# Kernel optimization log

Measured on AMD Instinct MI355X. Metric: run time of the kernel, lower is better.

Reference implementation:

```python
import jax, jax.numpy as jnp
import numpy as np

S, L, T, E, H = 512, 5, 20, 768, 64


def setup_inputs() -> dict:
    key = jax.random.key(0)
    ks = jax.random.split(key, 32)

    def p(k, shape, scale=0.05):
        return jax.random.normal(k, shape, dtype=jnp.float32) * scale

    return {
        "text_input": jax.random.normal(ks[0], (S, L, T, E), dtype=jnp.float32),
        "time_inputs": jax.random.uniform(ks[1], (S, L, T), dtype=jnp.float32),
        # TimeLSTM per-stock params (gate order f, i, o, c_tmp)
        "Wall": p(ks[2], (S, H, 4 * H)), "bWall": p(ks[3], (S, 4 * H)),
        "Uall": p(ks[4], (S, E, 4 * H)), "bUall": p(ks[5], (S, 4 * H)),
        "Wd": p(ks[6], (S, H, H)), "bWd": p(ks[7], (S, H)),
        # shared text/day Attention per stock
        "W1": p(ks[8], (S, H, H)), "b1": p(ks[9], (S, H)),
        "W2": p(ks[10], (S, H, H)), "b2": p(ks[11], (S, H)),
        "V": p(ks[12], (S, H, 1)), "bV": p(ks[13], (S, 1)),
        # day nn.LSTM per stock (gate order i, f, g, o)
        "Wih": p(ks[14], (S, H, 4 * H)), "Whh": p(ks[15], (S, H, 4 * H)),
        "bih": p(ks[16], (S, 4 * H)), "bhh": p(ks[17], (S, 4 * H)),
        # shared output head
        "lin_w": p(ks[18], (H, 1)), "lin_b": p(ks[19], (1,)),
        "no_stocks": S,
    }


def _forward(text_input, time_inputs, Wall, bWall, Uall, bUall, Wd, bWd,
             W1, b1, W2, b2, V, bV, Wih, Whh, bih, bhh, lin_w, lin_b, no_stocks):
    def per_stock(x, ts, Wall, bWall, Uall, bUall, Wd, bWd,
                  W1, b1, W2, b2, V, bV, Wih, Whh, bih, bhh):
        # x: [L, T, E], ts: [L, T] -- lookback days are an inner batch for the TimeLSTM
        u = jnp.einsum('lte,eg->ltg', x, Uall) + bUall  # [L, T, 4H]

        def step(carry, inp):
            h, c = carry                 # [L, H]
            u_t, ts_t = inp              # [L, 4H], [L]
            c_s1 = jnp.tanh(c @ Wd + bWd)
            c_adj = (c - c_s1) + c_s1 * ts_t[:, None]
            gates = h @ Wall + bWall + u_t
            f, i, o, c_tmp = jnp.split(gates, 4, axis=1)
            f = jax.nn.sigmoid(f)
            i = jax.nn.sigmoid(i)
            o = jax.nn.sigmoid(o)
            c_tmp = jax.nn.sigmoid(c_tmp)  # sigmoid (not tanh), faithful to source
            c_new = f * c_adj + i * c_tmp
            h_new = o * jnp.tanh(c_new)
            return (h_new, c_new), o     # module collects the o gate as 'outputs'

        init = (jnp.zeros((L, H), x.dtype), jnp.zeros((L, H), x.dtype))
        (h_fin, _), o_seq = jax.lax.scan(step, init, (u.transpose(1, 0, 2), ts.T))
        full = o_seq.transpose(1, 0, 2)  # [L, T, H]

        # text attention: score = V(tanh(W1(last) + W2(full))), softmax over T
        score = jnp.tanh((h_fin @ W1 + b1)[:, None, :] + full @ W2 + b2) @ V + bV  # [L, T, 1]
        aw = jax.nn.softmax(score, axis=1)
        text_vec = jnp.sum(aw * full, axis=1)  # [L, H]

        # day nn.LSTM: input (1, L, H) seq-first => one cell step with batch=L, zero state
        h0 = jnp.zeros((L, H), x.dtype)
        g = text_vec @ Wih + bih + h0 @ Whh + bhh
        gi, gf, gg, go = jnp.split(g, 4, axis=1)
        c_d = jax.nn.sigmoid(gi) * jnp.tanh(gg)  # f * c0 = 0
        h_d = jax.nn.sigmoid(go) * jnp.tanh(c_d)  # [L, H]; output == h_n here

        # day attention reuses the SAME text_attention weights; full == last == h_d
        s2 = jnp.tanh(h_d @ W1 + b1 + h_d @ W2 + b2) @ V + bV  # [L, 1]
        aw2 = jax.nn.softmax(s2, axis=0)
        return jnp.sum(aw2 * h_d, axis=0)  # [H]

    ft_vec = jax.vmap(per_stock)(text_input, time_inputs, Wall, bWall, Uall, bUall,
                                 Wd, bWd, W1, b1, W2, b2, V, bV,
                                 Wih, Whh, bih, bhh)  # [S, H]
    return jax.nn.leaky_relu(ft_vec @ lin_w + lin_b, negative_slope=0.01)  # [S, 1]


def reference(text_input, time_inputs, Wall, bWall, Uall, bUall, Wd, bWd,
              W1, b1, W2, b2, V, bV, Wih, Whh, bih, bhh, lin_w, lin_b, no_stocks):
    return _forward(text_input, time_inputs, Wall, bWall, Uall, bUall, Wd, bWd,
                    W1, b1, W2, b2, V, bV, Wih, Whh, bih, bhh, lin_w, lin_b, no_stocks)
```

## Files before the change

### kernel.cpp

```cpp
#include <hip/hip_runtime.h>
#include <cstddef>

#define NS 512
#define NL 5
#define NT 20
#define NE 768
#define NH 64
#define NG 256

__device__ __forceinline__ float sigf(float x) { return 1.0f / (1.0f + expf(-x)); }

typedef __fp16 h16x2 __attribute__((ext_vector_type(2)));
typedef _Float16 f16x8 __attribute__((ext_vector_type(8)));
typedef __attribute__((ext_vector_type(4))) float f32x4;

union PkU { h16x2 h; unsigned u; };
union U16 { __fp16 f; unsigned short s; };

__device__ __forceinline__ void split_pk(float a, float b, unsigned& hi, unsigned& lo) {
    PkU H, L;
    H.h = __builtin_amdgcn_cvt_pkrtz(a, b);
    float ra = a - (float)H.h[0];
    float rb = b - (float)H.h[1];
    L.h = __builtin_amdgcn_cvt_pkrtz(ra, rb);
    hi = H.u; lo = L.u;
}

__device__ __forceinline__ void pack8(const float v[8], uint4& ph, uint4& pl) {
    split_pk(v[0], v[1], ph.x, pl.x);
    split_pk(v[2], v[3], ph.y, pl.y);
    split_pk(v[4], v[5], ph.z, pl.z);
    split_pk(v[6], v[7], ph.w, pl.w);
}

__device__ __forceinline__ void stage8(const float v[8], unsigned short* base, unsigned off) {
    uint4 ph, pl;
    pack8(v, ph, pl);
    *(uint4*)&base[off]       = ph;
    *(uint4*)&base[off + 512] = pl;
}

__global__ __launch_bounds__(512, 4) void k_gemm_u(
    const float* __restrict__ x, const float* __restrict__ U,
    const float* __restrict__ bU, float* __restrict__ u)
{
    __shared__ unsigned short Af[8 * 2 * 512];
    __shared__ unsigned short Bf[8 * 2 * 512];
    const int bid = blockIdx.x;
    const int s = bid >> 1, half = bid & 1;
    const int tid = threadIdx.x;
    const int wave = tid >> 6, lane = tid & 63;
    const int wm = wave & 1, wn = wave >> 1;
    const float* xg = x + (size_t)s * (NL * NT * NE);
    const float* Ug = U + (size_t)s * (NE * NG) + half * 128;

    f32x4 acc[4][2] = {};

    const int arow = tid >> 2, ab = tid & 3;
    const unsigned a_off = ((unsigned)(arow >> 4) * 2) * 512 + ((arow & 15) + 16 * ab) * 8;
    const int bcol = tid & 127, bkq = tid >> 7;
    const unsigned b_off = ((unsigned)(bcol >> 4) * 2) * 512 + ((bcol & 15) + 16 * bkq) * 8;

    float av[8], bv[8];
    {
        const float* pa = xg + (size_t)arow * NE + ab * 8;
        if (arow < 100) {
            float4 q0 = *(const float4*)pa, q1 = *(const float4*)(pa + 4);
            av[0]=q0.x; av[1]=q0.y; av[2]=q0.z; av[3]=q0.w;
            av[4]=q1.x; av[5]=q1.y; av[6]=q1.z; av[7]=q1.w;
        } else {
            #pragma unroll
            for (int j = 0; j < 8; ++j) av[j] = 0.0f;
        }
        #pragma unroll
        for (int j = 0; j < 8; ++j)
            bv[j] = Ug[(size_t)(8 * bkq + j) * NG + bcol];
    }

    for (int st = 0; st < 24; ++st) {
        stage8(av, Af, a_off);
        stage8(bv, Bf, b_off);
        __syncthreads();

        if (st + 1 < 24) {
            const int k0 = (st + 1) * 32;
            const float* pa = xg + (size_t)arow * NE + k0 + ab * 8;
            if (arow < 100) {
                float4 q0 = *(const float4*)pa, q1 = *(const float4*)(pa + 4);
                av[0]=q0.x; av[1]=q0.y; av[2]=q0.z; av[3]=q0.w;
                av[4]=q1.x; av[5]=q1.y; av[6]=q1.z; av[7]=q1.w;
            } else {
                #pragma unroll
                for (int j = 0; j < 8; ++j) av[j] = 0.0f;
            }
            #pragma unroll
            for (int j = 0; j < 8; ++j)
                bv[j] = Ug[(size_t)(k0 + 8 * bkq + j) * NG + bcol];
        }

        f16x8 bh[2], bl[2];
        #pragma unroll
        for (int ni = 0; ni < 2; ++ni) {
            const unsigned nt = wn * 2 + ni;
            bh[ni] = *(const f16x8*)&Bf[(nt * 2 + 0) * 512 + lane * 8];
            bl[ni] = *(const f16x8*)&Bf[(nt * 2 + 1) * 512 + lane * 8];
        }
        #pragma unroll
        for (int mi = 0; mi < 4; ++mi) {
            const unsigned mt = wm * 4 + mi;
            f16x8 ah = *(const f16x8*)&Af[(mt * 2 + 0) * 512 + lane * 8];
            f16x8 al = *(const f16x8*)&Af[(mt * 2 + 1) * 512 + lane * 8];
            #pragma unroll
            for (int ni = 0; ni < 2; ++ni) {
                acc[mi][ni] = __builtin_amdgcn_mfma_f32_16x16x32_f16(ah, bh[ni], acc[mi][ni], 0, 0, 0);
                acc[mi][ni] = __builtin_amdgcn_mfma_f32_16x16x32_f16(ah, bl[ni], acc[mi][ni], 0, 0, 0);
                acc[mi][ni] = __builtin_amdgcn_mfma_f32_16x16x32_f16(al, bh[ni], acc[mi][ni], 0, 0, 0);
            }
        }
        __syncthreads();
    }

    const int c_sub = 4 * (lane >> 4);
    #pragma unroll
    for (int ni = 0; ni < 2; ++ni) {
        const int gcol = half * 128 + (wn * 2 + ni) * 16 + (lane & 15);
        const float bb = bU[(size_t)s * NG + gcol];
        #pragma unroll
        for (int mi = 0; mi < 4; ++mi) {
            const int grow0 = wm * 64 + mi * 16 + c_sub;
            #pragma unroll
            for (int r = 0; r < 4; ++r) {
                const int grow = grow0 + r;
                if (grow < 100) {
                    const int ld = grow / 20, td = grow % 20;
                    u[(((size_t)s * NT + td) * NL + ld) * NG + gcol] = acc[mi][ni][r] + bb;
                }
            }
        }
    }
}

#define RSTRIDE 72

__global__ __launch_bounds__(512, 4) void k_recur(
    float* __restrict__ u, const float* __restrict__ ti,
    const float* __restrict__ Wall, const float* __restrict__ bWall,
    const float* __restrict__ Wd, const float* __restrict__ bWd)
{
    __shared__ float GATES[NL * NG];
    __shared__ float WDC[NL * NH];
    __shared__ unsigned short HSH[16 * RSTRIDE];
    __shared__ unsigned short HSL[16 * RSTRIDE];
    __shared__ unsigned short CSH[16 * RSTRIDE];
    __shared__ unsigned short CSL[16 * RSTRIDE];
    __shared__ float TSH[NL * NT];

    const int s = blockIdx.x;
    const int tid = threadIdx.x;
    const int wave = tid >> 6, lane = tid & 63;
    float* ug = u + (size_t)s * NT * NL * NG;

    for (int i = tid; i < 16 * RSTRIDE; i += 512) {
        HSH[i] = 0; HSL[i] = 0; CSH[i] = 0; CSL[i] = 0;
    }
    if (tid < NL * NT) TSH[tid] = ti[(size_t)s * NL * NT + tid];

    const int nT = (wave < 4) ? 3 : 2;
    f16x8 Bh[3][2], Bl[3][2];
    {
        const float* Wg = Wall + (size_t)s * (NH * NG);
        const float* Dg = Wd + (size_t)s * (NH * NH);
        const int fcol = lane & 15, foct = lane >> 4;
        #pragma unroll
        for (int t2 = 0; t2 < 3; ++t2) {
            if (t2 < nT) {
                const int tc = wave + t2 * 8;
                #pragma unroll
                for (int ks = 0; ks < 2; ++ks) {
                    float v[8];
                    if (tc < 16) {
                        #pragma unroll
                        for (int j = 0; j < 8; ++j)
                            v[j] = Wg[(size_t)(ks * 32 + foct * 8 + j) * NG + tc * 16 + fcol];
                    } else {
                        #pragma unroll
                        for (int j = 0; j < 8; ++j)
                            v[j] = Dg[(size_t)(ks * 32 + foct * 8 + j) * NH + (tc - 16) * 16 + fcol];
                    }
                    union { uint4 u4; f16x8 h8; } H, L;
                    pack8(v, H.u4, L.u4);
                    Bh[t2][ks] = H.h8;
                    Bl[t2][ks] = L.h8;
                }
            }
        }
    }

    const int lq = tid >> 6, hh = tid & 63;
    float bw[4], bwd_r = 0.0f, un[4], c_reg = 0.0f, h_reg = 0.0f;
    if (tid < 320) {
        #pragma unroll
        for (int j = 0; j < 4; ++j) {
            bw[j] = bWall[(size_t)s * NG + j * 64 + hh];
            un[j] = ug[(size_t)(0 * NL + lq) * NG + j * 64 + hh];
        }
        bwd_r = bWd[(size_t)s * NH + hh];
    }
    __syncthreads();

    const int arow = lane & 15, akq = lane >> 4;
    const unsigned afrag0 = (unsigned)arow * RSTRIDE + akq * 8;
    const unsigned afrag1 = afrag0 + 32;
    for (int t = 0; t < NT; ++t) {
        f16x8 ah[2], al[2];
        ah[0] = *(const f16x8*)&HSH[afrag0];
        ah[1] = *(const f16x8*)&HSH[afrag1];
        al[0] = *(const f16x8*)&HSL[afrag0];
        al[1] = *(const f16x8*)&HSL[afrag1];
        f16x8 cah[2], cal[2];
        if (wave < 4) {
            cah[0] = *(const f16x8*)&CSH[afrag0];
            cah[1] = *(const f16x8*)&CSH[afrag1];
            cal[0] = *(const f16x8*)&CSL[afrag0];
            cal[1] = *(const f16x8*)&CSL[afrag1];
        }
        #pragma unroll
        for (int t2 = 0; t2 < 3; ++t2) {
            if (t2 < nT) {
                const int tc = wave + t2 * 8;
                const bool isWd = (tc >= 16);
                f32x4 acc = {};
                #pragma unroll
                for (int ks = 0; ks < 2; ++ks) {
                    f16x8 A_h = isWd ? cah[ks] : ah[ks];
                    f16x8 A_l = isWd ? cal[ks] : al[ks];
                    acc = __builtin_amdgcn_mfma_f32_16x16x32_f16(A_h, Bh[t2][ks], acc, 0, 0, 0);
                    acc = __builtin_amdgcn_mfma_f32_16x16x32_f16(A_h, Bl[t2][ks], acc, 0, 0, 0);
                    acc = __builtin_amdgcn_mfma_f32_16x16x32_f16(A_l, Bh[t2][ks], acc, 0, 0, 0);
                }
                #pragma unroll
                for (int r = 0; r < 4; ++r) {
                    const int row = 4 * akq + r;
                    if (row < NL) {
                        if (!isWd) GATES[row * NG + tc * 16 + arow] = acc[r];
                        else       WDC[row * NH + (tc - 16) * 16 + arow] = acc[r];
                    }
                }
            }
        }
        float unx[4];
        if (tid < 320 && t + 1 < NT) {
            #pragma unroll
            for (int j = 0; j < 4; ++j)
                unx[j] = ug[(size_t)((t + 1) * NL + lq) * NG + j * 64 + hh];
        }
        __syncthreads();

        if (tid < 320) {
            float g0 = GATES[lq * NG + hh]        + bw[0] + un[0];
            float g1 = GATES[lq * NG + 64 + hh]   + bw[1] + un[1];
            float g2 = GATES[lq * NG + 128 + hh]  + bw[2] + un[2];
            float g3 = GATES[lq * NG + 192 + hh]  + bw[3] + un[3];
            float f  = sigf(g0), ii = sigf(g1), oo = sigf(g2), ct = sigf(g3);
            float cs1 = tanhf(WDC[lq * NH + hh] + bwd_r);
            float ca  = c_reg - cs1 + cs1 * TSH[lq * NT + t];
            float cn  = f * ca + ii * ct;
            c_reg = cn;
            h_reg = oo * tanhf(cn);
            const unsigned sidx = (unsigned)lq * RSTRIDE + hh;
            U16 a, b;
            a.f = (__fp16)h_reg;            HSH[sidx] = a.s;
            b.f = (__fp16)(h_reg - (float)a.f); HSL[sidx] = b.s;
            a.f = (__fp16)cn;               CSH[sidx] = a.s;
            b.f = (__fp16)(cn - (float)a.f);   CSL[sidx] = b.s;
            ug[(size_t)(t * NL + lq) * NG + hh] = oo;
            #pragma unroll
            for (int j = 0; j < 4; ++j) un[j] = unx[j];
        }
        __syncthreads();
    }
    if (tid < 320)
        ug[(size_t)(0 * NL + lq) * NG + 64 + hh] = h_reg;
}

#define P_W1    0
#define P_W2    4096
#define P_FULLO 8192
#define P_HS    14592
#define P_TQ    14912
#define P_CA    15232
#define P_SC    15552
#define P_B0    15652
#define P_B1    15716
#define P_BVV   15780
#define P_BV1   15844
#define P_TOT   15848

__global__ __launch_bounds__(320, 2) void k_post(
    const float* __restrict__ u,
    const float* __restrict__ W1, const float* __restrict__ b1,
    const float* __restrict__ W2, const float* __restrict__ b2,
    const float* __restrict__ V, const float* __restrict__ bV,
    const float* __restrict__ Wih, const float* __restrict__ bih,
    const float* __restrict__ bhh, const float* __restrict__ lin_w,
    const float* __restrict__ lin_b, float* __restrict__ out)
{
    __shared__ float sm[P_TOT];
    const int s = blockIdx.x;
    const int tid = threadIdx.x;
    const int lq = tid >> 6, hh = tid & 63;
    const int lane = hh;
    const float* ug = u + (size_t)s * NT * NL * NG;

    for (int i = tid; i < 1024; i += 320)
        *(float4*)&sm[P_W1 + i * 4] = *(const float4*)(W1 + (size_t)s * 4096 + i * 4);
    for (int i = tid; i < 1024; i += 320)
        *(float4*)&sm[P_W2 + i * 4] = *(const float4*)(W2 + (size_t)s * 4096 + i * 4);
    for (int i = tid; i < 1600; i += 320) {
        const int idx = i >> 4;
        const int l = idx / NT, t = idx % NT;
        const int k4 = (i & 15) * 4;
        *(float4*)&sm[P_FULLO + idx * NH + k4] =
            *(const float4*)(ug + (size_t)(t * NL + l) * NG + k4);
    }
    sm[P_HS + tid] = ug[(size_t)(0 * NL + lq) * NG + 64 + hh];
    if (tid < NH) {
        sm[P_B0 + tid]  = b1[(size_t)s * NH + tid];
        sm[P_B1 + tid]  = b2[(size_t)s * NH + tid];
        sm[P_BVV + tid] = V[(size_t)s * NH + tid];
    }
    if (tid == 0) sm[P_BV1] = bV[s];
    __syncthreads();

    {
        float qv = sm[P_B0 + hh];
        for (int k4 = 0; k4 < NH; k4 += 4) {
            float4 hv = *(const float4*)&sm[P_HS + lq * NH + k4];
            qv += hv.x * sm[P_W1 + (k4 + 0) * NH + hh]
                + hv.y * sm[P_W1 + (k4 + 1) * NH + hh]
                + hv.z * sm[P_W1 + (k4 + 2) * NH + hh]
                + hv.w * sm[P_W1 + (k4 + 3) * NH + hh];
        }
        sm[P_TQ + tid] = qv;
    }
    __syncthreads();

    for (int lt = lq; lt < NL * NT; lt += 5) {
        int l = lt / NT;
        float v = sm[P_TQ + l * NH + lane] + sm[P_B1 + lane];
        for (int k4 = 0; k4 < NH; k4 += 4) {
            float4 fv = *(const float4*)&sm[P_FULLO + lt * NH + k4];
            v += fv.x * sm[P_W2 + (k4 + 0) * NH + lane]
               + fv.y * sm[P_W2 + (k4 + 1) * NH + lane]
               + fv.z * sm[P_W2 + (k4 + 2) * NH + lane]
               + fv.w * sm[P_W2 + (k4 + 3) * NH + lane];
        }
        v = tanhf(v) * sm[P_BVV + lane];
        #pragma unroll
        for (int m = 32; m > 0; m >>= 1) v += __shfl_xor(v, m, 64);
        if (lane == 0) sm[P_SC + lt] = v + sm[P_BV1];
    }
    __syncthreads();

    if (tid < NL) {
        float mx = -1e30f;
        for (int t = 0; t < NT; ++t) mx = fmaxf(mx, sm[P_SC + tid * NT + t]);
        float sum = 0.0f;
        for (int t = 0; t < NT; ++t) {
            float e = expf(sm[P_SC + tid * NT + t] - mx);
            sm[P_SC + tid * NT + t] = e;
            sum += e;
        }
        float inv = 1.0f / sum;
        for (int t = 0; t < NT; ++t) sm[P_SC + tid * NT + t] *= inv;
    }
    __syncthreads();

    {
        float sv = 0.0f;
        #pragma unroll
        for (int t = 0; t < NT; ++t)
            sv += sm[P_SC + lq * NT + t] * sm[P_FULLO + (lq * NT + t) * NH + hh];
        sm[P_CA + tid] = sv;
    }
    __syncthreads();

    if (tid < NG) {
        float bsum = bih[(size_t)s * NG + tid] + bhh[(size_t)s * NG + tid];
        float d[NL];
        #pragma unroll
        for (int l = 0; l < NL; ++l) d[l] = bsum;
        for (int k = 0; k < NH; ++k) {
            float wk = Wih[((size_t)s * NH + k) * NG + tid];
            #pragma unroll
            for (int l = 0; l < NL; ++l)
                d[l] += sm[P_CA + l * NH + k] * wk;
        }
        #pragma unroll
        for (int l = 0; l < NL; ++l)
            sm[P_FULLO + l * NG + tid] = d[l];
    }
    __syncthreads();
    {
        float gi = sm[P_FULLO + lq * NG + hh];
        float gg = sm[P_FULLO + lq * NG + 128 + hh];
        float go = sm[P_FULLO + lq * NG + 192 + hh];
        float cd = sigf(gi) * tanhf(gg);
        sm[P_TQ + tid] = sigf(go) * tanhf(cd);
    }
    __syncthreads();

    {
        float v = sm[P_B0 + lane] + sm[P_B1 + lane];
        for (int k4 = 0; k4 < NH; k4 += 4) {
            float4 hv = *(const float4*)&sm[P_TQ + lq * NH + k4];
            v += hv.x * (sm[P_W1 + (k4 + 0) * NH + lane] + sm[P_W2 + (k4 + 0) * NH + lane])
               + hv.y * (sm[P_W1 + (k4 + 1) * NH + lane] + sm[P_W2 + (k4 + 1) * NH + lane])
               + hv.z * (sm[P_W1 + (k4 + 2) * NH + lane] + sm[P_W2 + (k4 + 2) * NH + lane])
               + hv.w * (sm[P_W1 + (k4 + 3) * NH + lane] + sm[P_W2 + (k4 + 3) * NH + lane]);
        }
        v = tanhf(v) * sm[P_BVV + lane];
        #pragma unroll
        for (int m = 32; m > 0; m >>= 1) v += __shfl_xor(v, m, 64);
        if (lane == 0) sm[P_SC + lq] = v + sm[P_BV1];
    }
    __syncthreads();
    if (tid == 0) {
        float mx = -1e30f;
        for (int l = 0; l < NL; ++l) mx = fmaxf(mx, sm[P_SC + l]);
        float sum = 0.0f;
        for (int l = 0; l < NL; ++l) {
            float e = expf(sm[P_SC + l] - mx);
            sm[P_SC + l] = e;
            sum += e;
        }
        float inv = 1.0f / sum;
        for (int l = 0; l < NL; ++l) sm[P_SC + l] *= inv;
    }
    __syncthreads();

    if (tid < NH) {
        float fv = 0.0f;
        #pragma unroll
        for (int l = 0; l < NL; ++l)
            fv += sm[P_SC + l] * sm[P_TQ + l * NH + tid];
        fv *= lin_w[tid];
        #pragma unroll
        for (int m = 32; m > 0; m >>= 1) fv += __shfl_xor(fv, m, 64);
        if (tid == 0) {
            float val = fv + lin_b[0];
            out[s] = val > 0.0f ? val : 0.01f * val;
        }
    }
}

extern "C" void kernel_launch(void* const* d_in, const int* in_sizes, int n_in,
                              void* d_out, int out_size, void* d_ws, size_t ws_size,
                              hipStream_t stream) {
    (void)in_sizes; (void)n_in; (void)out_size; (void)ws_size;
    const float* x     = (const float*)d_in[0];
    const float* ti    = (const float*)d_in[1];
    const float* Wall  = (const float*)d_in[2];
    const float* bWall = (const float*)d_in[3];
    const float* Uall  = (const float*)d_in[4];
    const float* bUall = (const float*)d_in[5];
    const float* Wd    = (const float*)d_in[6];
    const float* bWd   = (const float*)d_in[7];
    const float* W1    = (const float*)d_in[8];
    const float* b1    = (const float*)d_in[9];
    const float* W2    = (const float*)d_in[10];
    const float* b2    = (const float*)d_in[11];
    const float* V     = (const float*)d_in[12];
    const float* bV    = (const float*)d_in[13];
    const float* Wih   = (const float*)d_in[14];
    const float* bih   = (const float*)d_in[16];
    const float* bhh   = (const float*)d_in[17];
    const float* lin_w = (const float*)d_in[18];
    const float* lin_b = (const float*)d_in[19];
    float* out = (float*)d_out;
    float* u = (float*)d_ws;

    k_gemm_u<<<NS * 2, 512, 0, stream>>>(x, Uall, bUall, u);
    k_recur<<<NS, 512, 0, stream>>>(u, ti, Wall, bWall, Wd, bWd);
    k_post<<<NS, 320, 0, stream>>>(u, W1, b1, W2, b2, V, bV,
                                   Wih, bih, bhh, lin_w, lin_b, out);
}
```

Baseline: 831.8 us.

## Fuse recurrence and attention/day-LSTM post-processing into one kernel

Merges the TimeLSTM recurrence kernel with the post-processing kernel, so each block keeps the per-step output gates and final hidden state in shared memory instead of writing them to the global workspace and reading them back. This removes one launch and the global round trip for those intermediates. Shared memory per block grows a lot (W1, W2 and FULLO arrays on top of the recurrence state), which can cut how many blocks fit per CU. The post-processing now runs on 512-thread blocks with some threads idle.

Result: faster. 788.3 us (-5.2%).

```diff
diff --git a/kernel.cpp b/kernel.cpp
--- a/kernel.cpp
+++ b/kernel.cpp
@@ -7,6 +7,7 @@
 #define NE 768
 #define NH 64
 #define NG 256
+#define RSTRIDE 72
 
 __device__ __forceinline__ float sigf(float x) { return 1.0f / (1.0f + expf(-x)); }
 
@@ -140,30 +141,52 @@
     }
 }
 
-#define RSTRIDE 72
-
-__global__ __launch_bounds__(512, 4) void k_recur(
-    float* __restrict__ u, const float* __restrict__ ti,
+__global__ __launch_bounds__(512, 4) void k_fused(
+    const float* __restrict__ u, const float* __restrict__ ti,
     const float* __restrict__ Wall, const float* __restrict__ bWall,
-    const float* __restrict__ Wd, const float* __restrict__ bWd)
+    const float* __restrict__ Wd, const float* __restrict__ bWd,
+    const float* __restrict__ W1, const float* __restrict__ b1,
+    const float* __restrict__ W2, const float* __restrict__ b2,
+    const float* __restrict__ V, const float* __restrict__ bV,
+    const float* __restrict__ Wih, const float* __restrict__ bih,
+    const float* __restrict__ bhh, const float* __restrict__ lin_w,
+    const float* __restrict__ lin_b, float* __restrict__ out)
 {
+    __shared__ float FW1[4096];
+    __shared__ float FW2[4096];
+    __shared__ float FULLO[NL * NT * NH];
     __shared__ float GATES[NL * NG];
     __shared__ float WDC[NL * NH];
+    __shared__ float TSH[NL * NT];
+    __shared__ float PHS[320];
+    __shared__ float PTQ[320];
+    __shared__ float PCA[320];
+    __shared__ float PSC[100];
+    __shared__ float PB0[64], PB1[64], PBVV[64], PBV1[1];
     __shared__ unsigned short HSH[16 * RSTRIDE];
     __shared__ unsigned short HSL[16 * RSTRIDE];
     __shared__ unsigned short CSH[16 * RSTRIDE];
     __shared__ unsigned short CSL[16 * RSTRIDE];
-    __shared__ float TSH[NL * NT];
 
     const int s = blockIdx.x;
     const int tid = threadIdx.x;
     const int wave = tid >> 6, lane = tid & 63;
-    float* ug = u + (size_t)s * NT * NL * NG;
-
+    const float* ug = u + (size_t)s * NT * NL * NG;
+
+    for (int i = tid; i < 1024; i += 512)
+        *(float4*)&FW1[i * 4] = *(const float4*)(W1 + (size_t)s * 4096 + i * 4);
+    for (int i = tid; i < 1024; i += 512)
+        *(float4*)&FW2[i * 4] = *(const float4*)(W2 + (size_t)s * 4096 + i * 4);
     for (int i = tid; i < 16 * RSTRIDE; i += 512) {
         HSH[i] = 0; HSL[i] = 0; CSH[i] = 0; CSL[i] = 0;
     }
     if (tid < NL * NT) TSH[tid] = ti[(size_t)s * NL * NT + tid];
+    if (tid < NH) {
+        PB0[tid]  = b1[(size_t)s * NH + tid];
+        PB1[tid]  = b2[(size_t)s * NH + tid];
+        PBVV[tid] = V[(size_t)s * NH + tid];
+    }
+    if (tid == 0) PBV1[0] = bV[s];
 
     const int nT = (wave < 4) ? 3 : 2;
     f16x8 Bh[3][2], Bl[3][2];
@@ -197,6 +220,7 @@
     }
 
     const int lq = tid >> 6, hh = tid & 63;
+    const int lane64 = hh;
     float bw[4], bwd_r = 0.0f, un[4], c_reg = 0.0f, h_reg = 0.0f;
     if (tid < 320) {
         #pragma unroll
@@ -269,119 +293,69 @@
             h_reg = oo * tanhf(cn);
             const unsigned sidx = (unsigned)lq * RSTRIDE + hh;
             U16 a, b;
-            a.f = (__fp16)h_reg;            HSH[sidx] = a.s;
+            a.f = (__fp16)h_reg;               HSH[sidx] = a.s;
             b.f = (__fp16)(h_reg - (float)a.f); HSL[sidx] = b.s;
-            a.f = (__fp16)cn;               CSH[sidx] = a.s;
+            a.f = (__fp16)cn;                  CSH[sidx] = a.s;
             b.f = (__fp16)(cn - (float)a.f);   CSL[sidx] = b.s;
-            ug[(size_t)(t * NL + lq) * NG + hh] = oo;
+            FULLO[(lq * NT + t) * NH + hh] = oo;
             #pragma unroll
             for (int j = 0; j < 4; ++j) un[j] = unx[j];
         }
         __syncthreads();
     }
-    if (tid < 320)
-        ug[(size_t)(0 * NL + lq) * NG + 64 + hh] = h_reg;
-}
-
-#define P_W1    0
-#define P_W2    4096
-#define P_FULLO 8192
-#define P_HS    14592
-#define P_TQ    14912
-#define P_CA    15232
-#define P_SC    15552
-#define P_B0    15652
-#define P_B1    15716
-#define P_BVV   15780
-#define P_BV1   15844
-#define P_TOT   15848
-
-__global__ __launch_bounds__(320, 2) void k_post(
-    const float* __restrict__ u,
-    const float* __restrict__ W1, const float* __restrict__ b1,
-    const float* __restrict__ W2, const float* __restrict__ b2,
-    const float* __restrict__ V, const float* __restrict__ bV,
-    const float* __restrict__ Wih, const float* __restrict__ bih,
-    const float* __restrict__ bhh, const float* __restrict__ lin_w,
-    const float* __restrict__ lin_b, float* __restrict__ out)
-{
-    __shared__ float sm[P_TOT];
-    const int s = blockIdx.x;
-    const int tid = threadIdx.x;
-    const int lq = tid >> 6, hh = tid & 63;
-    const int lane = hh;
-    const float* ug = u + (size_t)s * NT * NL * NG;
-
-    for (int i = tid; i < 1024; i += 320)
-        *(float4*)&sm[P_W1 + i * 4] = *(const float4*)(W1 + (size_t)s * 4096 + i * 4);
-    for (int i = tid; i < 1024; i += 320)
-        *(float4*)&sm[P_W2 + i * 4] = *(const float4*)(W2 + (size_t)s * 4096 + i * 4);
-    for (int i = tid; i < 1600; i += 320) {
-        const int idx = i >> 4;
-        const int l = idx / NT, t = idx % NT;
-        const int k4 = (i & 15) * 4;
-        *(float4*)&sm[P_FULLO + idx * NH + k4] =
-            *(const float4*)(ug + (size_t)(t * NL + l) * NG + k4);
-    }
-    sm[P_HS + tid] = ug[(size_t)(0 * NL + lq) * NG + 64 + hh];
-    if (tid < NH) {
-        sm[P_B0 + tid]  = b1[(size_t)s * NH + tid];
-        sm[P_B1 + tid]  = b2[(size_t)s * NH + tid];
-        sm[P_BVV + tid] = V[(size_t)s * NH + tid];
-    }
-    if (tid == 0) sm[P_BV1] = bV[s];
-    __syncthreads();
-
-    {
-        float qv = sm[P_B0 + hh];
+    if (tid < 320) PHS[tid] = h_reg;
+    __syncthreads();
+
+    if (tid < 320) {
+        float qv = PB0[hh];
         for (int k4 = 0; k4 < NH; k4 += 4) {
-            float4 hv = *(const float4*)&sm[P_HS + lq * NH + k4];
-            qv += hv.x * sm[P_W1 + (k4 + 0) * NH + hh]
-                + hv.y * sm[P_W1 + (k4 + 1) * NH + hh]
-                + hv.z * sm[P_W1 + (k4 + 2) * NH + hh]
-                + hv.w * sm[P_W1 + (k4 + 3) * NH + hh];
-        }
-        sm[P_TQ + tid] = qv;
-    }
-    __syncthreads();
-
-    for (int lt = lq; lt < NL * NT; lt += 5) {
+            float4 hv = *(const float4*)&PHS[lq * NH + k4];
+            qv += hv.x * FW1[(k4 + 0) * NH + hh]
+                + hv.y * FW1[(k4 + 1) * NH + hh]
+                + hv.z * FW1[(k4 + 2) * NH + hh]
+                + hv.w * FW1[(k4 + 3) * NH + hh];
+        }
+        PTQ[tid] = qv;
+    }
+    __syncthreads();
+
+    for (int lt = wave; lt < NL * NT; lt += 8) {
         int l = lt / NT;
-        float v = sm[P_TQ + l * NH + lane] + sm[P_B1 + lane];
+        float v = PTQ[l * NH + lane64] + PB1[lane64];
         for (int k4 = 0; k4 < NH; k4 += 4) {
-            float4 fv = *(const float4*)&sm[P_FULLO + lt * NH + k4];
-            v += fv.x * sm[P_W2 + (k4 + 0) * NH + lane]
-               + fv.y * sm[P_W2 + (k4 + 1) * NH + lane]
-               + fv.z * sm[P_W2 + (k4 + 2) * NH + lane]
-               + fv.w * sm[P_W2 + (k4 + 3) * NH + lane];
-        }
-        v = tanhf(v) * sm[P_BVV + lane];
+            float4 fv = *(const float4*)&FULLO[lt * NH + k4];
+            v += fv.x * FW2[(k4 + 0) * NH + lane64]
+               + fv.y * FW2[(k4 + 1) * NH + lane64]
+               + fv.z * FW2[(k4 + 2) * NH + lane64]
+               + fv.w * FW2[(k4 + 3) * NH + lane64];
+        }
+        v = tanhf(v) * PBVV[lane64];
         #pragma unroll
         for (int m = 32; m > 0; m >>= 1) v += __shfl_xor(v, m, 64);
-        if (lane == 0) sm[P_SC + lt] = v + sm[P_BV1];
+        if (lane64 == 0) PSC[lt] = v + PBV1[0];
     }
     __syncthreads();
 
     if (tid < NL) {
         float mx = -1e30f;
-        for (int t = 0; t < NT; ++t) mx = fmaxf(mx, sm[P_SC + tid * NT + t]);
+        for (int t = 0; t < NT; ++t) mx = fmaxf(mx, PSC[tid * NT + t]);
         float sum = 0.0f;
         for (int t = 0; t < NT; ++t) {
-            float e = expf(sm[P_SC + tid * NT + t] - mx);
-            sm[P_SC + tid * NT + t] = e;
+            float e = expf(PSC[tid * NT + t] - mx);
+            PSC[tid * NT + t] = e;
             sum += e;
         }
         float inv = 1.0f / sum;
-        for (int t = 0; t < NT; ++t) sm[P_SC + tid * NT + t] *= inv;
-    }
-    __syncthreads();
-
-    {
+        for (int t = 0; t < NT; ++t) PSC[tid * NT + t] *= inv;
+    }
+    __syncthreads();
+
+    if (tid < 320) {
         float sv = 0.0f;
         #pragma unroll
         for (int t = 0; t < NT; ++t)
-            sv += sm[P_SC + lq * NT + t] * sm[P_FULLO + (lq * NT + t) * NH + hh];
-        sm[P_CA + tid] = sv;
+            sv += PSC[lq * NT + t] * FULLO[(lq * NT + t) * NH + hh];
+        PCA[tid] = sv;
     }
     __syncthreads();
 
@@ -394,48 +368,48 @@
             float wk = Wih[((size_t)s * NH + k) * NG + tid];
             #pragma unroll
             for (int l = 0; l < NL; ++l)
-                d[l] += sm[P_CA + l * NH + k] * wk;
+                d[l] += PCA[l * NH + k] * wk;
         }
         #pragma unroll
         for (int l = 0; l < NL; ++l)
-            sm[P_FULLO + l * NG + tid] = d[l];
-    }
-    __syncthreads();
-    {
-        float gi = sm[P_FULLO + lq * NG + hh];
-        float gg = sm[P_FULLO + lq * NG + 128 + hh];
-        float go = sm[P_FULLO + lq * NG + 192 + hh];
+            FULLO[l * NG + tid] = d[l];
+    }
+    __syncthreads();
+    if (tid < 320) {
+        float gi = FULLO[lq * NG + hh];
+        float gg = FULLO[lq * NG + 128 + hh];
+        float go = FULLO[lq * NG + 192 + hh];
         float cd = sigf(gi) * tanhf(gg);
-        sm[P_TQ + tid] = sigf(go) * tanhf(cd);
-    }
-    __syncthreads();
-
-    {
-        float v = sm[P_B0 + lane] + sm[P_B1 + lane];
+        PTQ[tid] = sigf(go) * tanhf(cd);
+    }
+    __syncthreads();
+
+    if (lq < NL) {
+        float v = PB0[lane64] + PB1[lane64];
         for (int k4 = 0; k4 < NH; k4 += 4) {
-            float4 hv = *(const float4*)&sm[P_TQ + lq * NH + k4];
-            v += hv.x * (sm[P_W1 + (k4 + 0) * NH + lane] + sm[P_W2 + (k4 + 0) * NH + lane])
-               + hv.y * (sm[P_W1 + (k4 + 1) * NH + lane] + sm[P_W2 + (k4 + 1) * NH + lane])
-               + hv.z * (sm[P_W1 + (k4 + 2) * NH + lane] + sm[P_W2 + (k4 + 2) * NH + lane])
-               + hv.w * (sm[P_W1 + (k4 + 3) * NH + lane] + sm[P_W2 + (k4 + 3) * NH + lane]);
-        }
-        v = tanhf(v) * sm[P_BVV + lane];
+            float4 hv = *(const float4*)&PTQ[lq * NH + k4];
+            v += hv.x * (FW1[(k4 + 0) * NH + lane64] + FW2[(k4 + 0) * NH + lane64])
+               + hv.y * (FW1[(k4 + 1) * NH + lane64] + FW2[(k4 + 1) * NH + lane64])
+               + hv.z * (FW1[(k4 + 2) * NH + lane64] + FW2[(k4 + 2) * NH + lane64])
+               + hv.w * (FW1[(k4 + 3) * NH + lane64] + FW2[(k4 + 3) * NH + lane64]);
+        }
+        v = tanhf(v) * PBVV[lane64];
         #pragma unroll
         for (int m = 32; m > 0; m >>= 1) v += __shfl_xor(v, m, 64);
-        if (lane == 0) sm[P_SC + lq] = v + sm[P_BV1];
+        if (lane64 == 0) PSC[lq] = v + PBV1[0];
     }
     __syncthreads();
     if (tid == 0) {
         float mx = -1e30f;
-        for (int l = 0; l < NL; ++l) mx = fmaxf(mx, sm[P_SC + l]);
+        for (int l = 0; l < NL; ++l) mx = fmaxf(mx, PSC[l]);
         float sum = 0.0f;
         for (int l = 0; l < NL; ++l) {
-            float e = expf(sm[P_SC + l] - mx);
-            sm[P_SC + l] = e;
+            float e = expf(PSC[l] - mx);
+            PSC[l] = e;
             sum += e;
         }
         float inv = 1.0f / sum;
-        for (int l = 0; l < NL; ++l) sm[P_SC + l] *= inv;
+        for (int l = 0; l < NL; ++l) PSC[l] *= inv;
     }
     __syncthreads();
 
@@ -443,7 +417,7 @@
         float fv = 0.0f;
         #pragma unroll
         for (int l = 0; l < NL; ++l)
-            fv += sm[P_SC + l] * sm[P_TQ + l * NH + tid];
+            fv += PSC[l] * PTQ[l * NH + tid];
         fv *= lin_w[tid];
         #pragma unroll
         for (int m = 32; m > 0; m >>= 1) fv += __shfl_xor(fv, m, 64);
@@ -481,7 +455,7 @@
     float* u = (float*)d_ws;
 
     k_gemm_u<<<NS * 2, 512, 0, stream>>>(x, Uall, bUall, u);
-    k_recur<<<NS, 512, 0, stream>>>(u, ti, Wall, bWall, Wd, bWd);
-    k_post<<<NS, 320, 0, stream>>>(u, W1, b1, W2, b2, V, bV,
-                                   Wih, bih, bhh, lin_w, lin_b, out);
-}
+    k_fused<<<NS, 512, 0, stream>>>(u, ti, Wall, bWall, Wd, bWd,
+                                    W1, b1, W2, b2, V, bV,
+                                    Wih, bih, bhh, lin_w, lin_b, out);
+}
```
